# Kernel optimization log

Hardware: AMD Instinct MI355X
Metric: run time of the kernel (lower is better)

## Reference

```python
import jax, jax.numpy as jnp
import numpy as np

N, E, F_IN, C, H = 50000, 800000, 256, 64, 2  # nodes, edges, in-feat, per-head dim, heads
NEG_SLOPE_ATT = 0.2   # GATConv leaky_relu slope
NEG_SLOPE = 0.01      # F.leaky_relu default
BN_EPS = 1e-5


def setup_inputs() -> dict:
    key = jax.random.key(0)
    ks = jax.random.split(key, 10)
    x = jax.random.normal(ks[0], (N, F_IN), dtype=jnp.float32)
    edge_index = jax.random.randint(ks[1], (2, E), 0, N, dtype=jnp.int32)
    # GATConv params
    W = jax.random.normal(ks[2], (F_IN, H * C), dtype=jnp.float32) / np.sqrt(F_IN)
    att_src = jax.random.normal(ks[3], (H, C), dtype=jnp.float32) / np.sqrt(C)
    att_dst = jax.random.normal(ks[4], (H, C), dtype=jnp.float32) / np.sqrt(C)
    conv_bias = jnp.zeros((H * C,), dtype=jnp.float32)
    # fc1: in = hidden*2*2 = 256, out = hidden = 64
    fc1_w = jax.random.normal(ks[5], (H * C * 2, C), dtype=jnp.float32) / np.sqrt(H * C * 2)
    fc1_b = jnp.zeros((C,), dtype=jnp.float32)
    bn_gamma = jnp.ones((C,), dtype=jnp.float32)
    bn_beta = jnp.zeros((C,), dtype=jnp.float32)
    bn_mean = jnp.zeros((C,), dtype=jnp.float32)
    bn_var = jnp.ones((C,), dtype=jnp.float32)
    fc2_w = jax.random.normal(ks[6], (C, 3), dtype=jnp.float32) / np.sqrt(C)
    fc2_b = jnp.zeros((3,), dtype=jnp.float32)
    return {"x": x, "edge_index": edge_index, "W": W, "att_src": att_src,
            "att_dst": att_dst, "conv_bias": conv_bias, "fc1_w": fc1_w, "fc1_b": fc1_b,
            "bn_gamma": bn_gamma, "bn_beta": bn_beta, "bn_mean": bn_mean,
            "bn_var": bn_var, "fc2_w": fc2_w, "fc2_b": fc2_b}


def gat_conv(x, edge_index, W, att_src, att_dst, bias):
    # Project: [N, H, C]
    h = (x @ W).reshape(N, H, C)
    a_s = jnp.einsum('nhc,hc->nh', h, att_src)  # [N, H]
    a_d = jnp.einsum('nhc,hc->nh', h, att_dst)
    # add self-loops (PyG default)
    loops = jnp.arange(N, dtype=edge_index.dtype)
    src = jnp.concatenate([edge_index[0], loops])
    dst = jnp.concatenate([edge_index[1], loops])
    e = jax.nn.leaky_relu(a_s[src] + a_d[dst], NEG_SLOPE_ATT)  # [E+N, H]
    # segment softmax over incoming edges of each dst node
    m = jax.ops.segment_max(e, dst, num_segments=N)
    e_exp = jnp.exp(e - m[dst])
    denom = jax.ops.segment_sum(e_exp, dst, num_segments=N)
    alpha = e_exp / denom[dst]  # [E+N, H]
    msg = h[src] * alpha[:, :, None]  # [E+N, H, C]
    out = jax.ops.segment_sum(msg, dst, num_segments=N)  # [N, H, C]
    return out.reshape(N, H * C) + bias


def reference(x, edge_index, W, att_src, att_dst, conv_bias, fc1_w, fc1_b,
              bn_gamma, bn_beta, bn_mean, bn_var, fc2_w, fc2_b):
    # eval mode: dropout = identity, BN uses running stats
    h = gat_conv(x, edge_index, W, att_src, att_dst, conv_bias)
    h = jax.nn.leaky_relu(h, NEG_SLOPE)
    edge_rep = jnp.concatenate([h[edge_index[0]], h[edge_index[1]]], axis=1)  # [E, 256]
    y = edge_rep @ fc1_w + fc1_b
    y = (y - bn_mean) * jax.lax.rsqrt(bn_var + BN_EPS) * bn_gamma + bn_beta
    y = jax.nn.leaky_relu(y, NEG_SLOPE)
    return y @ fc2_w + fc2_b  # [E, 3]
```

## Files before the change

### kernel.cpp

```cpp
#include <hip/hip_runtime.h>
#include <hip/hip_bf16.h>

#define N_NODES 50000
#define N_EDGES 800000
#define F_IN    256
#define C_DIM   64
#define HC      128
#define NPG     6250
#define NBB     32
#define NBLK    196

typedef __attribute__((ext_vector_type(8))) short bf16x8;
typedef __attribute__((ext_vector_type(4))) float f32x4;

static constexpr size_t OFF_HBF   = 0;
static constexpr size_t OFF_H2    = 12800000;
static constexpr size_t OFF_AB    = 25600000;
static constexpr size_t OFF_AS    = 38400000;
static constexpr size_t OFF_AD    = 38800000;
static constexpr size_t OFF_OFFS  = 39200000;
static constexpr size_t OFF_TOT   = 39400064;
static constexpr size_t OFF_CUR   = 39600064;
static constexpr size_t OFF_PART  = 39800064;
static constexpr size_t OFF_CSR2  = 39801088;
static constexpr size_t OFF_WT    = 46201088;
static constexpr size_t OFF_FC1T  = 46266624;
static constexpr size_t OFF_SCALE = 46299392;
static constexpr size_t OFF_CC    = 46299904;
static constexpr size_t OFF_FC2M  = 46300416;
static constexpr size_t OFF_BCNT  = 46302464;
static constexpr size_t OFF_BASE  = 52702464;

__device__ __forceinline__ float2 bf2(unsigned u) {
    float2 r;
    r.x = __uint_as_float(u << 16);
    r.y = __uint_as_float(u & 0xffff0000u);
    return r;
}
__device__ __forceinline__ unsigned short f2bf(float f) {
    unsigned u = __float_as_uint(f);
    return (unsigned short)((u + 0x7fffu + ((u >> 16) & 1u)) >> 16);
}
__device__ __forceinline__ short f2bf_s(float f) {
    __hip_bfloat16 h = __float2bfloat16(f);
    return *reinterpret_cast<short*>(&h);
}

__global__ __launch_bounds__(256) void k_prep(const float* __restrict__ W,
                                              const float* __restrict__ fc1,
                                              const float* __restrict__ fc1_b,
                                              const float* __restrict__ gamma,
                                              const float* __restrict__ beta,
                                              const float* __restrict__ mean,
                                              const float* __restrict__ var,
                                              const float* __restrict__ fc2_w,
                                              unsigned short* __restrict__ Wt,
                                              unsigned short* __restrict__ fc1t,
                                              float* __restrict__ scale,
                                              float* __restrict__ cc,
                                              unsigned short* __restrict__ fc2m) {
    int id = blockIdx.x * 256 + threadIdx.x;
    if (id < 32768) {
        int n = id >> 8, k = id & 255;
        Wt[id] = f2bf(W[k * HC + n]);
    }
    int id2 = id - 32768;
    if (id2 >= 0 && id2 < 16384) {
        int j = id2 >> 7, q = id2 & 127;
        int L = q >> 1, b = q & 1;
        int kch = 32 * (L >> 4) + (L & 15) + 16 * b;
        float v = (j < 64) ? fc1[kch * 64 + j] : fc1[(128 + kch) * 64 + (j - 64)];
        fc1t[id2] = f2bf(v);
    }
    int id3 = id - (32768 + 16384);
    if (id3 >= 0 && id3 < 128) {
        int jj = id3 & 63;
        float s = gamma[jj] * rsqrtf(var[jj] + 1e-5f);
        scale[id3] = s;
        cc[id3] = (id3 < 64) ? 0.f : (fc1_b[jj] - mean[jj]) * s + beta[jj];
    }
    int id4 = id - (32768 + 16384 + 128);
    if (id4 >= 0 && id4 < 1024) {
        int kk = id4 >> 9, rem = id4 & 511;
        int lane = rem >> 3, j = rem & 7;
        int q  = kk * 16 + (lane >> 4) * 4 + (j >> 1);
        int ch = 32 * (q >> 4) + (q & 15) + 16 * (j & 1);
        int col = lane & 15;
        float v = (col < 3) ? fc2_w[ch * 3 + col] : 0.f;
        fc2m[id4] = f2bf(v);
    }
}

__global__ __launch_bounds__(256) void k_hist(const int* __restrict__ dst,
                                              int* __restrict__ bcnt) {
    __shared__ int hist[NPG];
    const int g  = blockIdx.x & 7;
    const int bi = blockIdx.x >> 3;
    const int lo = g * NPG, hi = lo + NPG;
    for (int j = threadIdx.x; j < NPG; j += 256) hist[j] = 0;
    __syncthreads();
    const int4* d4 = (const int4*)dst + bi * 6250;
#pragma unroll 1
    for (int it = 0; it < 25; ++it) {
        int idx = it * 256 + threadIdx.x;
        if (idx < 6250) {
            int4 d = d4[idx];
            if (d.x >= lo && d.x < hi) atomicAdd(&hist[d.x - lo], 1);
            if (d.y >= lo && d.y < hi) atomicAdd(&hist[d.y - lo], 1);
            if (d.z >= lo && d.z < hi) atomicAdd(&hist[d.z - lo], 1);
            if (d.w >= lo && d.w < hi) atomicAdd(&hist[d.w - lo], 1);
        }
    }
    __syncthreads();
    int* row = bcnt + (size_t)(g * NBB + bi) * NPG;
    for (int j = threadIdx.x; j < NPG; j += 256) row[j] = hist[j];
}

__global__ void k_tot(const int* __restrict__ bcnt, int* __restrict__ tot) {
    int n = blockIdx.x * 256 + threadIdx.x;
    if (n >= N_NODES) return;
    int g = n / NPG, ln = n - g * NPG;
    const int* col = bcnt + (size_t)g * NBB * NPG + ln;
    int s = 0;
#pragma unroll
    for (int bi = 0; bi < NBB; ++bi) s += col[bi * NPG];
    tot[n] = s;
}

__global__ void k_scan_part(const int* __restrict__ deg, int* __restrict__ part) {
    __shared__ int sd[256];
    int i = blockIdx.x * 256 + threadIdx.x;
    sd[threadIdx.x] = (i < N_NODES) ? deg[i] : 0;
    __syncthreads();
    for (int off = 128; off > 0; off >>= 1) {
        if (threadIdx.x < off) sd[threadIdx.x] += sd[threadIdx.x + off];
        __syncthreads();
    }
    if (threadIdx.x == 0) part[blockIdx.x] = sd[0];
}

__global__ void k_scan_final(const int* __restrict__ deg, const int* __restrict__ part,
                             int* __restrict__ offs) {
    __shared__ int sp[256];
    __shared__ int sd[256];
    const int t = threadIdx.x;
    int pv = (t < NBLK && t < (int)blockIdx.x) ? part[t] : 0;
    sp[t] = pv;
    __syncthreads();
    for (int off = 128; off > 0; off >>= 1) {
        if (t < off) sp[t] += sp[t + off];
        __syncthreads();
    }
    const int base = sp[0];
    __syncthreads();
    int i = blockIdx.x * 256 + t;
    int v = (i < N_NODES) ? deg[i] : 0;
    sd[t] = v;
    __syncthreads();
    for (int off = 1; off < 256; off <<= 1) {
        int u = (t >= off) ? sd[t - off] : 0;
        __syncthreads();
        sd[t] += u;
        __syncthreads();
    }
    if (i < N_NODES) {
        int o = base + sd[t] - v;
        offs[i] = o;
        if (i == N_NODES - 1) offs[N_NODES] = o + v;
    }
}

__global__ void k_base(const int* __restrict__ bcnt, const int* __restrict__ offs,
                       int* __restrict__ base) {
    int n = blockIdx.x * 256 + threadIdx.x;
    if (n >= N_NODES) return;
    int g = n / NPG, ln = n - g * NPG;
    const int* col = bcnt + (size_t)g * NBB * NPG + ln;
    int* bcol = base + (size_t)g * NBB * NPG + ln;
    int run = offs[n];
#pragma unroll
    for (int bi = 0; bi < NBB; ++bi) {
        bcol[bi * NPG] = run;
        run += col[bi * NPG];
    }
}

__global__ __launch_bounds__(256) void k_scatter(const int* __restrict__ src,
                                                 const int* __restrict__ dst,
                                                 const int* __restrict__ base,
                                                 int2* __restrict__ csr2) {
    __shared__ int cnt[NPG];
    const int g  = blockIdx.x & 7;
    const int bi = blockIdx.x >> 3;
    const int lo = g * NPG, hi = lo + NPG;
    const int* brow = base + (size_t)(g * NBB + bi) * NPG;
    for (int j = threadIdx.x; j < NPG; j += 256) cnt[j] = brow[j];
    __syncthreads();
    const int4* d4 = (const int4*)dst + bi * 6250;
    const int4* s4 = (const int4*)src + bi * 6250;
    const int ebase = bi * 25000;
#pragma unroll 1
    for (int it = 0; it < 25; ++it) {
        int idx = it * 256 + threadIdx.x;
        if (idx < 6250) {
            int4 d = d4[idx];
            int4 s = s4[idx];
            int e = ebase + idx * 4;
            if (d.x >= lo && d.x < hi) { int p = atomicAdd(&cnt[d.x - lo], 1); csr2[p] = make_int2(s.x, e);     }
            if (d.y >= lo && d.y < hi) { int p = atomicAdd(&cnt[d.y - lo], 1); csr2[p] = make_int2(s.y, e + 1); }
            if (d.z >= lo && d.z < hi) { int p = atomicAdd(&cnt[d.z - lo], 1); csr2[p] = make_int2(s.z, e + 2); }
            if (d.w >= lo && d.w < hi) { int p = atomicAdd(&cnt[d.w - lo], 1); csr2[p] = make_int2(s.w, e + 3); }
        }
    }
}

__global__ __launch_bounds__(256, 4) void k_mfma_xw(const float* __restrict__ x,
                                                    const unsigned short* __restrict__ Wt,
                                                    const float* __restrict__ att_src,
                                                    const float* __restrict__ att_dst,
                                                    unsigned* __restrict__ h_p,
                                                    float* __restrict__ as_,
                                                    float* __restrict__ ad_) {
    __shared__ float xs[16 * 256];
    __shared__ float sAs[16][2], sAd[16][2];
    const int t    = threadIdx.x;
    const int v    = t >> 6;
    const int lane = t & 63;
    const int c16  = lane & 15;
    const int kg   = lane >> 4;
    const int r0   = blockIdx.x * 16;
    if (t < 32) { ((float*)sAs)[t] = 0.f; ((float*)sAd)[t] = 0.f; }

    {
        const float4* xsrc = (const float4*)(x + (size_t)r0 * F_IN);
        float4* xsl = (float4*)xs;
#pragma unroll
        for (int it = 0; it < 4; ++it) {
            int cidx = it * 256 + t;
            int rl = cidx >> 6, j = cidx & 63;
            float4 val = xsrc[cidx];
            xsl[rl * 64 + (j ^ rl)] = val;
        }
    }
    const int cf0 = 2 * v, cf1 = 2 * v + 1;
    bf16x8 wf0[8], wf1[8];
#pragma unroll
    for (int kk = 0; kk < 8; ++kk) {
        wf0[kk] = *(const bf16x8*)(Wt + (size_t)(cf0 * 16 + c16) * 256 + kk * 32 + kg * 8);
        wf1[kk] = *(const bf16x8*)(Wt + (size_t)(cf1 * 16 + c16) * 256 + kk * 32 + kg * 8);
    }
    __syncthreads();

    f32x4 acc0 = {}, acc1 = {};
#pragma unroll
    for (int kk = 0; kk < 8; ++kk) {
        int j0 = kk * 8 + kg * 2;
        float4 a0 = *(const float4*)(xs + (size_t)(c16 * 64 + (j0 ^ c16)) * 4);
        float4 a1 = *(const float4*)(xs + (size_t)(c16 * 64 + ((j0 + 1) ^ c16)) * 4);
        float fv[8] = {a0.x, a0.y, a0.z, a0.w, a1.x, a1.y, a1.z, a1.w};
        bf16x8 ahi, alo;
#pragma unroll
        for (int q = 0; q < 8; ++q) {
            unsigned u = __float_as_uint(fv[q]);
            float hval = __uint_as_float(u & 0xffff0000u);
            float d = fv[q] - hval;
            ahi[q] = (short)(u >> 16);
            alo[q] = (short)(__float_as_uint(d) >> 16);
        }
        acc0 = __builtin_amdgcn_mfma_f32_16x16x32_bf16(alo, wf0[kk], acc0, 0, 0, 0);
        acc0 = __builtin_amdgcn_mfma_f32_16x16x32_bf16(ahi, wf0[kk], acc0, 0, 0, 0);
        acc1 = __builtin_amdgcn_mfma_f32_16x16x32_bf16(alo, wf1[kk], acc1, 0, 0, 0);
        acc1 = __builtin_amdgcn_mfma_f32_16x16x32_bf16(ahi, wf1[kk], acc1, 0, 0, 0);
    }
#pragma unroll
    for (int i = 0; i < 4; ++i) {
        int row = r0 + kg * 4 + i;
        unsigned pu = (unsigned)f2bf(acc0[i]) | ((unsigned)f2bf(acc1[i]) << 16);
        h_p[(size_t)row * 64 + v * 16 + c16] = pu;
    }
    float ws0 = att_src[cf0 * 16 + c16], ws1 = att_src[cf1 * 16 + c16];
    float wd0 = att_dst[cf0 * 16 + c16], wd1 = att_dst[cf1 * 16 + c16];
    float pas[4], pad[4];
#pragma unroll
    for (int i = 0; i < 4; ++i) {
        pas[i] = acc0[i] * ws0 + acc1[i] * ws1;
        pad[i] = acc0[i] * wd0 + acc1[i] * wd1;
    }
#pragma unroll
    for (int m = 1; m < 16; m <<= 1) {
#pragma unroll
        for (int i = 0; i < 4; ++i) {
            pas[i] += __shfl_xor(pas[i], m, 64);
            pad[i] += __shfl_xor(pad[i], m, 64);
        }
    }
    const int head = v >> 1;
    if (c16 == 0) {
#pragma unroll
        for (int i = 0; i < 4; ++i) {
            atomicAdd(&sAs[kg * 4 + i][head], pas[i]);
            atomicAdd(&sAd[kg * 4 + i][head], pad[i]);
        }
    }
    __syncthreads();
    if (t < 32) {
        int row = t >> 1, hd = t & 1;
        as_[(r0 + row) * 2 + hd] = sAs[row][hd];
        ad_[(r0 + row) * 2 + hd] = sAd[row][hd];
    }
}

__global__ __launch_bounds__(256) void k_agg(const unsigned* __restrict__ h_p,
                                             const float* __restrict__ as_,
                                             const float* __restrict__ ad_,
                                             const int* __restrict__ offs,
                                             const int2* __restrict__ csr2,
                                             const float* __restrict__ conv_bias,
                                             unsigned* __restrict__ h2_p) {
    const int n    = blockIdx.x * 4 + (threadIdx.x >> 6);
    const int lane = threadIdx.x & 63;
    const int ql   = lane & 15;
    const int q    = lane >> 4;
    const int hd   = ql >> 3;
    const float adn = ad_[n * 2 + hd];
    const uint4* h4 = (const uint4*)h_p;
    float a[8] = {};
    float accw = 0.f;
    const int beg = offs[n], end = offs[n + 1];
    int i = beg + q;
    for (; i + 4 < end; i += 8) {
        int s0 = csr2[i].x;
        int s1 = csr2[i + 4].x;
        uint4 u0 = h4[(unsigned)(s0 * 16 + ql)];
        uint4 u1 = h4[(unsigned)(s1 * 16 + ql)];
        float l0 = as_[s0 * 2 + hd] + adn;
        float l1 = as_[s1 * 2 + hd] + adn;
        l0 = fmaxf(l0, 0.2f * l0);
        l1 = fmaxf(l1, 0.2f * l1);
        float w0 = __expf(l0), w1 = __expf(l1);
        float2 t;
        t = bf2(u0.x); a[0] += w0 * t.x; a[1] += w0 * t.y;
        t = bf2(u0.y); a[2] += w0 * t.x; a[3] += w0 * t.y;
        t = bf2(u0.z); a[4] += w0 * t.x; a[5] += w0 * t.y;
        t = bf2(u0.w); a[6] += w0 * t.x; a[7] += w0 * t.y;
        t = bf2(u1.x); a[0] += w1 * t.x; a[1] += w1 * t.y;
        t = bf2(u1.y); a[2] += w1 * t.x; a[3] += w1 * t.y;
        t = bf2(u1.z); a[4] += w1 * t.x; a[5] += w1 * t.y;
        t = bf2(u1.w); a[6] += w1 * t.x; a[7] += w1 * t.y;
        accw += w0 + w1;
    }
    if (i < end) {
        int s0 = csr2[i].x;
        uint4 u0 = h4[(unsigned)(s0 * 16 + ql)];
        float l0 = as_[s0 * 2 + hd] + adn;
        l0 = fmaxf(l0, 0.2f * l0);
        float w0 = __expf(l0);
        float2 t;
        t = bf2(u0.x); a[0] += w0 * t.x; a[1] += w0 * t.y;
        t = bf2(u0.y); a[2] += w0 * t.x; a[3] += w0 * t.y;
        t = bf2(u0.z); a[4] += w0 * t.x; a[5] += w0 * t.y;
        t = bf2(u0.w); a[6] += w0 * t.x; a[7] += w0 * t.y;
        accw += w0;
    }
#pragma unroll
    for (int m = 16; m < 64; m <<= 1) {
#pragma unroll
        for (int j = 0; j < 8; ++j) a[j] += __shfl_xor(a[j], m, 64);
        accw += __shfl_xor(accw, m, 64);
    }
    if (q == 0) {
        float es = as_[n * 2 + hd] + adn;
        es = fmaxf(es, 0.2f * es);
        float wsl = __expf(es);
        uint4 un = h4[(unsigned)(n * 16 + ql)];
        float2 t;
        t = bf2(un.x); a[0] += wsl * t.x; a[1] += wsl * t.y;
        t = bf2(un.y); a[2] += wsl * t.x; a[3] += wsl * t.y;
        t = bf2(un.z); a[4] += wsl * t.x; a[5] += wsl * t.y;
        t = bf2(un.w); a[6] += wsl * t.x; a[7] += wsl * t.y;
        accw += wsl;
        float rinv = 1.f / accw;
        unsigned pw[4];
#pragma unroll
        for (int j = 0; j < 4; ++j) {
            int w = 4 * ql + j;
            int c = 32 * (w >> 4) + (w & 15);
            float o0 = a[2 * j] * rinv + conv_bias[c];
            float o1 = a[2 * j + 1] * rinv + conv_bias[c + 16];
            o0 = fmaxf(o0, 0.01f * o0);
            o1 = fmaxf(o1, 0.01f * o1);
            pw[j] = (unsigned)f2bf(o0) | ((unsigned)f2bf(o1) << 16);
        }
        ((uint4*)h2_p)[(unsigned)(n * 16 + ql)] = make_uint4(pw[0], pw[1], pw[2], pw[3]);
    }
}

__global__ __launch_bounds__(256) void k_mfma_uv(const unsigned short* __restrict__ h2,
                                                 const unsigned short* __restrict__ fc1t,
                                                 const float* __restrict__ scale,
                                                 const float* __restrict__ cc,
                                                 unsigned* __restrict__ ab_p) {
    const int w = blockIdx.x * 4 + (threadIdx.x >> 6);
    if (w >= N_NODES / 16) return;
    const int lane = threadIdx.x & 63;
    const int c16  = lane & 15;
    const int kg   = lane >> 4;
    const int r0   = w * 16;
    const unsigned short* arow = h2 + (size_t)(r0 + c16) * HC + kg * 8;
    bf16x8 af[4];
#pragma unroll
    for (int kk = 0; kk < 4; ++kk) af[kk] = *(const bf16x8*)(arow + kk * 32);
    f32x4 acc[8] = {};
#pragma unroll
    for (int kk = 0; kk < 4; ++kk) {
        const unsigned short* wp = fc1t + c16 * HC + kk * 32 + kg * 8;
#pragma unroll
        for (int cf = 0; cf < 8; ++cf) {
            bf16x8 b = *(const bf16x8*)(wp + cf * 16 * HC);
            acc[cf] = __builtin_amdgcn_mfma_f32_16x16x32_bf16(af[kk], b, acc[cf], 0, 0, 0);
        }
    }
#pragma unroll
    for (int cf = 0; cf < 8; cf += 2) {
        int j0 = cf * 16 + c16, j1 = j0 + 16;
        float s0 = scale[j0], s1 = scale[j1];
        float q0 = cc[j0],    q1 = cc[j1];
#pragma unroll
        for (int i = 0; i < 4; ++i) {
            int row = r0 + kg * 4 + i;
            unsigned pu = (unsigned)f2bf(acc[cf][i] * s0 + q0)
                        | ((unsigned)f2bf(acc[cf + 1][i] * s1 + q1) << 16);
            ab_p[(size_t)row * 64 + (cf >> 1) * 16 + c16] = pu;
        }
    }
}

__device__ __forceinline__ void mk_afrag(uint4 ua, const float* bb, bf16x8& ap) {
    float2 t; float z;
    t = bf2(ua.x);
    z = t.x + bb[0]; z = fmaxf(z, 0.01f * z); ap[0] = f2bf_s(z);
    z = t.y + bb[1]; z = fmaxf(z, 0.01f * z); ap[1] = f2bf_s(z);
    t = bf2(ua.y);
    z = t.x + bb[2]; z = fmaxf(z, 0.01f * z); ap[2] = f2bf_s(z);
    z = t.y + bb[3]; z = fmaxf(z, 0.01f * z); ap[3] = f2bf_s(z);
    t = bf2(ua.z);
    z = t.x + bb[4]; z = fmaxf(z, 0.01f * z); ap[4] = f2bf_s(z);
    z = t.y + bb[5]; z = fmaxf(z, 0.01f * z); ap[5] = f2bf_s(z);
    t = bf2(ua.w);
    z = t.x + bb[6]; z = fmaxf(z, 0.01f * z); ap[6] = f2bf_s(z);
    z = t.y + bb[7]; z = fmaxf(z, 0.01f * z); ap[7] = f2bf_s(z);
}

__global__ __launch_bounds__(256) void k_edge(const int* __restrict__ offs,
                                              const int2* __restrict__ csr2,
                                              const unsigned* __restrict__ ab_p,
                                              const unsigned short* __restrict__ fc2m,
                                              const float* __restrict__ fc2_b,
                                              float* __restrict__ out) {
    const int n    = blockIdx.x * 4 + (threadIdx.x >> 6);
    const int lane = threadIdx.x & 63;
    const int c16  = lane & 15;
    const int kg   = lane >> 4;
    bf16x8 bfr0 = *(const bf16x8*)(fc2m + (size_t)lane * 8);
    bf16x8 bfr1 = *(const bf16x8*)(fc2m + (size_t)(64 + lane) * 8);
    const uint4* abv = (const uint4*)ab_p;
    uint4 ub0 = abv[(unsigned)(n * 16 + 8 + kg)];
    uint4 ub1 = abv[(unsigned)(n * 16 + 12 + kg)];
    float bb0[8], bb1[8];
    {
        float2 t;
        t = bf2(ub0.x); bb0[0] = t.x; bb0[1] = t.y;
        t = bf2(ub0.y); bb0[2] = t.x; bb0[3] = t.y;
        t = bf2(ub0.z); bb0[4] = t.x; bb0[5] = t.y;
        t = bf2(ub0.w); bb0[6] = t.x; bb0[7] = t.y;
        t = bf2(ub1.x); bb1[0] = t.x; bb1[1] = t.y;
        t = bf2(ub1.y); bb1[2] = t.x; bb1[3] = t.y;
        t = bf2(ub1.z); bb1[4] = t.x; bb1[5] = t.y;
        t = bf2(ub1.w); bb1[6] = t.x; bb1[7] = t.y;
    }
    const float ob = (c16 < 3) ? fc2_b[c16] : 0.f;
    const int beg = offs[n], end = offs[n + 1];
    for (int base = beg; base < end; base += 16) {
        int slot = base + c16;
        int2 ce = (slot < end) ? csr2[slot] : make_int2(0, 0);
        uint4 ua0 = abv[(unsigned)(ce.x * 16 + kg)];
        uint4 ua1 = abv[(unsigned)(ce.x * 16 + 4 + kg)];
        bf16x8 ap0, ap1;
        mk_afrag(ua0, bb0, ap0);
        mk_afrag(ua1, bb1, ap1);
        f32x4 acc = {};
        acc = __builtin_amdgcn_mfma_f32_16x16x32_bf16(ap0, bfr0, acc, 0, 0, 0);
        acc = __builtin_amdgcn_mfma_f32_16x16x32_bf16(ap1, bfr1, acc, 0, 0, 0);
#pragma unroll
        for (int i = 0; i < 4; ++i) {
            int eid = __shfl(ce.y, kg * 4 + i, 64);
            if (c16 < 3 && (base + kg * 4 + i) < end)
                out[(size_t)eid * 3 + c16] = acc[i] + ob;
        }
    }
}

extern "C" void kernel_launch(void* const* d_in, const int* in_sizes, int n_in,
                              void* d_out, int out_size, void* d_ws, size_t ws_size,
                              hipStream_t stream) {
    const float* x        = (const float*)d_in[0];
    const int*   ei       = (const int*)d_in[1];
    const float* W        = (const float*)d_in[2];
    const float* att_src  = (const float*)d_in[3];
    const float* att_dst  = (const float*)d_in[4];
    const float* conv_b   = (const float*)d_in[5];
    const float* fc1_w    = (const float*)d_in[6];
    const float* fc1_b    = (const float*)d_in[7];
    const float* gamma    = (const float*)d_in[8];
    const float* beta     = (const float*)d_in[9];
    const float* mean     = (const float*)d_in[10];
    const float* var      = (const float*)d_in[11];
    const float* fc2_w    = (const float*)d_in[12];
    const float* fc2_b    = (const float*)d_in[13];
    float*       out      = (float*)d_out;
    char*        ws       = (char*)d_ws;

    const int* src = ei;
    const int* dst = ei + N_EDGES;

    unsigned*       h_p   = (unsigned*)(ws + OFF_HBF);
    unsigned*       h2_p  = (unsigned*)(ws + OFF_H2);
    unsigned*       ab_p  = (unsigned*)(ws + OFF_AB);
    float*          as_   = (float*)(ws + OFF_AS);
    float*          ad_   = (float*)(ws + OFF_AD);
    int*            offs  = (int*)(ws + OFF_OFFS);
    int*            tot   = (int*)(ws + OFF_TOT);
    int*            part  = (int*)(ws + OFF_PART);
    int2*           csr2  = (int2*)(ws + OFF_CSR2);
    unsigned short* Wt    = (unsigned short*)(ws + OFF_WT);
    unsigned short* fc1t  = (unsigned short*)(ws + OFF_FC1T);
    float*          scale = (float*)(ws + OFF_SCALE);
    float*          cc    = (float*)(ws + OFF_CC);
    unsigned short* fc2m  = (unsigned short*)(ws + OFF_FC2M);
    int*            bcnt  = (int*)(ws + OFF_BCNT);
    int*            base  = (int*)(ws + OFF_BASE);

    k_prep<<<235, 256, 0, stream>>>(W, fc1_w, fc1_b, gamma, beta, mean, var, fc2_w,
                                    Wt, fc1t, scale, cc, fc2m);

    k_hist      <<<8 * NBB, 256, 0, stream>>>(dst, bcnt);
    k_tot       <<<NBLK, 256, 0, stream>>>(bcnt, tot);
    k_scan_part <<<NBLK, 256, 0, stream>>>(tot, part);
    k_scan_final<<<NBLK, 256, 0, stream>>>(tot, part, offs);
    k_base      <<<NBLK, 256, 0, stream>>>(bcnt, offs, base);
    k_scatter   <<<8 * NBB, 256, 0, stream>>>(src, dst, base, csr2);

    k_mfma_xw<<<N_NODES / 16, 256, 0, stream>>>(x, Wt, att_src, att_dst, h_p, as_, ad_);
    k_agg    <<<N_NODES / 4, 256, 0, stream>>>(h_p, as_, ad_, offs, csr2, conv_b, h2_p);
    k_mfma_uv<<<(N_NODES / 16 + 3) / 4, 256, 0, stream>>>((const unsigned short*)h2_p, fc1t, scale, cc, ab_p);

    k_edge<<<N_NODES / 4, 256, 0, stream>>>(offs, csr2, ab_p, fc2m, fc2_b, out);
}
```

Measured before the change: 172.2 us.

## Merge histogram into XW GEMM launch and fuse scan kernels

The edge-destination histogram blocks are folded into the XW projection kernel as extra blocks of a single launch, so the two independent stages can run concurrently on the GPU. The total-degree reduction is merged with the partial-scan kernel, and the per-bucket base computation is merged with the final scan. Together these cut the launch count from 8 to 4 for this front section and remove intermediate kernel boundaries. The trade-off is a heterogeneous kernel whose shared-memory footprint is the larger of the two roles, which may lower occupancy for the GEMM blocks.

```diff
diff --git a/kernel.cpp b/kernel.cpp
--- a/kernel.cpp
+++ b/kernel.cpp
@@ -9,6 +9,8 @@
 #define NPG     6250
 #define NBB     32
 #define NBLK    196
+#define XW_BLOCKS   3125
+#define HIST_BLOCKS 256
 
 typedef __attribute__((ext_vector_type(8))) short bf16x8;
 typedef __attribute__((ext_vector_type(4))) float f32x4;
@@ -20,7 +22,6 @@
 static constexpr size_t OFF_AD    = 38800000;
 static constexpr size_t OFF_OFFS  = 39200000;
 static constexpr size_t OFF_TOT   = 39400064;
-static constexpr size_t OFF_CUR   = 39600064;
 static constexpr size_t OFF_PART  = 39800064;
 static constexpr size_t OFF_CSR2  = 39801088;
 static constexpr size_t OFF_WT    = 46201088;
@@ -91,46 +92,145 @@
     }
 }
 
-__global__ __launch_bounds__(256) void k_hist(const int* __restrict__ dst,
-                                              int* __restrict__ bcnt) {
-    __shared__ int hist[NPG];
-    const int g  = blockIdx.x & 7;
-    const int bi = blockIdx.x >> 3;
-    const int lo = g * NPG, hi = lo + NPG;
-    for (int j = threadIdx.x; j < NPG; j += 256) hist[j] = 0;
-    __syncthreads();
-    const int4* d4 = (const int4*)dst + bi * 6250;
+__global__ __launch_bounds__(256, 4) void k_front(const float* __restrict__ x,
+                                                  const unsigned short* __restrict__ Wt,
+                                                  const float* __restrict__ att_src,
+                                                  const float* __restrict__ att_dst,
+                                                  unsigned* __restrict__ h_p,
+                                                  float* __restrict__ as_,
+                                                  float* __restrict__ ad_,
+                                                  const int* __restrict__ dst,
+                                                  int* __restrict__ bcnt) {
+    __shared__ int smem[6464];
+    const int t = threadIdx.x;
+
+    if (blockIdx.x >= XW_BLOCKS) {
+        int* hist = smem;
+        const int bid = blockIdx.x - XW_BLOCKS;
+        const int g  = bid & 7;
+        const int bi = bid >> 3;
+        const int lo = g * NPG, hi = lo + NPG;
+        for (int j = t; j < NPG; j += 256) hist[j] = 0;
+        __syncthreads();
+        const int4* d4 = (const int4*)dst + bi * 6250;
 #pragma unroll 1
-    for (int it = 0; it < 25; ++it) {
-        int idx = it * 256 + threadIdx.x;
-        if (idx < 6250) {
-            int4 d = d4[idx];
-            if (d.x >= lo && d.x < hi) atomicAdd(&hist[d.x - lo], 1);
-            if (d.y >= lo && d.y < hi) atomicAdd(&hist[d.y - lo], 1);
-            if (d.z >= lo && d.z < hi) atomicAdd(&hist[d.z - lo], 1);
-            if (d.w >= lo && d.w < hi) atomicAdd(&hist[d.w - lo], 1);
-        }
-    }
-    __syncthreads();
-    int* row = bcnt + (size_t)(g * NBB + bi) * NPG;
-    for (int j = threadIdx.x; j < NPG; j += 256) row[j] = hist[j];
-}
-
-__global__ void k_tot(const int* __restrict__ bcnt, int* __restrict__ tot) {
+        for (int it = 0; it < 25; ++it) {
+            int idx = it * 256 + t;
+            if (idx < 6250) {
+                int4 d = d4[idx];
+                if (d.x >= lo && d.x < hi) atomicAdd(&hist[d.x - lo], 1);
+                if (d.y >= lo && d.y < hi) atomicAdd(&hist[d.y - lo], 1);
+                if (d.z >= lo && d.z < hi) atomicAdd(&hist[d.z - lo], 1);
+                if (d.w >= lo && d.w < hi) atomicAdd(&hist[d.w - lo], 1);
+            }
+        }
+        __syncthreads();
+        int* row = bcnt + (size_t)(g * NBB + bi) * NPG;
+        for (int j = t; j < NPG; j += 256) row[j] = hist[j];
+        return;
+    }
+
+    float* xs  = (float*)smem;
+    float* sAs = (float*)(smem + 4096);
+    float* sAd = sAs + 32;
+    const int v    = t >> 6;
+    const int lane = t & 63;
+    const int c16  = lane & 15;
+    const int kg   = lane >> 4;
+    const int r0   = blockIdx.x * 16;
+    if (t < 32) { sAs[t] = 0.f; sAd[t] = 0.f; }
+    {
+        const float4* xsrc = (const float4*)(x + (size_t)r0 * F_IN);
+        float4* xsl = (float4*)xs;
+#pragma unroll
+        for (int it = 0; it < 4; ++it) {
+            int cidx = it * 256 + t;
+            int rl = cidx >> 6, j = cidx & 63;
+            float4 val = xsrc[cidx];
+            xsl[rl * 64 + (j ^ rl)] = val;
+        }
+    }
+    const int cf0 = 2 * v, cf1 = 2 * v + 1;
+    bf16x8 wf0[8], wf1[8];
+#pragma unroll
+    for (int kk = 0; kk < 8; ++kk) {
+        wf0[kk] = *(const bf16x8*)(Wt + (size_t)(cf0 * 16 + c16) * 256 + kk * 32 + kg * 8);
+        wf1[kk] = *(const bf16x8*)(Wt + (size_t)(cf1 * 16 + c16) * 256 + kk * 32 + kg * 8);
+    }
+    __syncthreads();
+
+    f32x4 acc0 = {}, acc1 = {};
+#pragma unroll
+    for (int kk = 0; kk < 8; ++kk) {
+        int j0 = kk * 8 + kg * 2;
+        float4 a0 = *(const float4*)(xs + (size_t)(c16 * 64 + (j0 ^ c16)) * 4);
+        float4 a1 = *(const float4*)(xs + (size_t)(c16 * 64 + ((j0 + 1) ^ c16)) * 4);
+        float fv[8] = {a0.x, a0.y, a0.z, a0.w, a1.x, a1.y, a1.z, a1.w};
+        bf16x8 ahi, alo;
+#pragma unroll
+        for (int q = 0; q < 8; ++q) {
+            unsigned u = __float_as_uint(fv[q]);
+            float hval = __uint_as_float(u & 0xffff0000u);
+            float d = fv[q] - hval;
+            ahi[q] = (short)(u >> 16);
+            alo[q] = (short)(__float_as_uint(d) >> 16);
+        }
+        acc0 = __builtin_amdgcn_mfma_f32_16x16x32_bf16(alo, wf0[kk], acc0, 0, 0, 0);
+        acc0 = __builtin_amdgcn_mfma_f32_16x16x32_bf16(ahi, wf0[kk], acc0, 0, 0, 0);
+        acc1 = __builtin_amdgcn_mfma_f32_16x16x32_bf16(alo, wf1[kk], acc1, 0, 0, 0);
+        acc1 = __builtin_amdgcn_mfma_f32_16x16x32_bf16(ahi, wf1[kk], acc1, 0, 0, 0);
+    }
+#pragma unroll
+    for (int i = 0; i < 4; ++i) {
+        int row = r0 + kg * 4 + i;
+        unsigned pu = (unsigned)f2bf(acc0[i]) | ((unsigned)f2bf(acc1[i]) << 16);
+        h_p[(size_t)row * 64 + v * 16 + c16] = pu;
+    }
+    float ws0 = att_src[cf0 * 16 + c16], ws1 = att_src[cf1 * 16 + c16];
+    float wd0 = att_dst[cf0 * 16 + c16], wd1 = att_dst[cf1 * 16 + c16];
+    float pas[4], pad[4];
+#pragma unroll
+    for (int i = 0; i < 4; ++i) {
+        pas[i] = acc0[i] * ws0 + acc1[i] * ws1;
+        pad[i] = acc0[i] * wd0 + acc1[i] * wd1;
+    }
+#pragma unroll
+    for (int m = 1; m < 16; m <<= 1) {
+#pragma unroll
+        for (int i = 0; i < 4; ++i) {
+            pas[i] += __shfl_xor(pas[i], m, 64);
+            pad[i] += __shfl_xor(pad[i], m, 64);
+        }
+    }
+    const int head = v >> 1;
+    if (c16 == 0) {
+#pragma unroll
+        for (int i = 0; i < 4; ++i) {
+            atomicAdd(&sAs[(kg * 4 + i) * 2 + head], pas[i]);
+            atomicAdd(&sAd[(kg * 4 + i) * 2 + head], pad[i]);
+        }
+    }
+    __syncthreads();
+    if (t < 32) {
+        int row = t >> 1, hd = t & 1;
+        as_[(r0 + row) * 2 + hd] = sAs[row * 2 + hd];
+        ad_[(r0 + row) * 2 + hd] = sAd[row * 2 + hd];
+    }
+}
+
+__global__ void k_tot_part(const int* __restrict__ bcnt, int* __restrict__ tot,
+                           int* __restrict__ part) {
+    __shared__ int sd[256];
     int n = blockIdx.x * 256 + threadIdx.x;
-    if (n >= N_NODES) return;
-    int g = n / NPG, ln = n - g * NPG;
-    const int* col = bcnt + (size_t)g * NBB * NPG + ln;
     int s = 0;
-#pragma unroll
-    for (int bi = 0; bi < NBB; ++bi) s += col[bi * NPG];
-    tot[n] = s;
-}
-
-__global__ void k_scan_part(const int* __restrict__ deg, int* __restrict__ part) {
-    __shared__ int sd[256];
-    int i = blockIdx.x * 256 + threadIdx.x;
-    sd[threadIdx.x] = (i < N_NODES) ? deg[i] : 0;
+    if (n < N_NODES) {
+        int g = n / NPG, ln = n - g * NPG;
+        const int* col = bcnt + (size_t)g * NBB * NPG + ln;
+#pragma unroll
+        for (int bi = 0; bi < NBB; ++bi) s += col[bi * NPG];
+        tot[n] = s;
+    }
+    sd[threadIdx.x] = s;
     __syncthreads();
     for (int off = 128; off > 0; off >>= 1) {
         if (threadIdx.x < off) sd[threadIdx.x] += sd[threadIdx.x + off];
@@ -139,8 +239,9 @@
     if (threadIdx.x == 0) part[blockIdx.x] = sd[0];
 }
 
-__global__ void k_scan_final(const int* __restrict__ deg, const int* __restrict__ part,
-                             int* __restrict__ offs) {
+__global__ void k_scan_base(const int* __restrict__ tot, const int* __restrict__ part,
+                            const int* __restrict__ bcnt, int* __restrict__ offs,
+                            int* __restrict__ base) {
     __shared__ int sp[256];
     __shared__ int sd[256];
     const int t = threadIdx.x;
@@ -151,10 +252,10 @@
         if (t < off) sp[t] += sp[t + off];
         __syncthreads();
     }
-    const int base = sp[0];
+    const int bb = sp[0];
     __syncthreads();
     int i = blockIdx.x * 256 + t;
-    int v = (i < N_NODES) ? deg[i] : 0;
+    int v = (i < N_NODES) ? tot[i] : 0;
     sd[t] = v;
     __syncthreads();
     for (int off = 1; off < 256; off <<= 1) {
@@ -164,24 +265,18 @@
         __syncthreads();
     }
     if (i < N_NODES) {
-        int o = base + sd[t] - v;
+        int o = bb + sd[t] - v;
         offs[i] = o;
         if (i == N_NODES - 1) offs[N_NODES] = o + v;
-    }
-}
-
-__global__ void k_base(const int* __restrict__ bcnt, const int* __restrict__ offs,
-                       int* __restrict__ base) {
-    int n = blockIdx.x * 256 + threadIdx.x;
-    if (n >= N_NODES) return;
-    int g = n / NPG, ln = n - g * NPG;
-    const int* col = bcnt + (size_t)g * NBB * NPG + ln;
-    int* bcol = base + (size_t)g * NBB * NPG + ln;
-    int run = offs[n];
-#pragma unroll
-    for (int bi = 0; bi < NBB; ++bi) {
-        bcol[bi * NPG] = run;
-        run += col[bi * NPG];
+        int g = i / NPG, ln = i - g * NPG;
+        const int* col = bcnt + (size_t)g * NBB * NPG + ln;
+        int* bcol = base + (size_t)g * NBB * NPG + ln;
+        int run = o;
+#pragma unroll
+        for (int bi = 0; bi < NBB; ++bi) {
+            bcol[bi * NPG] = run;
+            run += col[bi * NPG];
+        }
     }
 }
 
@@ -211,102 +306,6 @@
             if (d.z >= lo && d.z < hi) { int p = atomicAdd(&cnt[d.z - lo], 1); csr2[p] = make_int2(s.z, e + 2); }
             if (d.w >= lo && d.w < hi) { int p = atomicAdd(&cnt[d.w - lo], 1); csr2[p] = make_int2(s.w, e + 3); }
         }
-    }
-}
-
-__global__ __launch_bounds__(256, 4) void k_mfma_xw(const float* __restrict__ x,
-                                                    const unsigned short* __restrict__ Wt,
-                                                    const float* __restrict__ att_src,
-                                                    const float* __restrict__ att_dst,
-                                                    unsigned* __restrict__ h_p,
-                                                    float* __restrict__ as_,
-                                                    float* __restrict__ ad_) {
-    __shared__ float xs[16 * 256];
-    __shared__ float sAs[16][2], sAd[16][2];
-    const int t    = threadIdx.x;
-    const int v    = t >> 6;
-    const int lane = t & 63;
-    const int c16  = lane & 15;
-    const int kg   = lane >> 4;
-    const int r0   = blockIdx.x * 16;
-    if (t < 32) { ((float*)sAs)[t] = 0.f; ((float*)sAd)[t] = 0.f; }
-
-    {
-        const float4* xsrc = (const float4*)(x + (size_t)r0 * F_IN);
-        float4* xsl = (float4*)xs;
-#pragma unroll
-        for (int it = 0; it < 4; ++it) {
-            int cidx = it * 256 + t;
-            int rl = cidx >> 6, j = cidx & 63;
-            float4 val = xsrc[cidx];
-            xsl[rl * 64 + (j ^ rl)] = val;
-        }
-    }
-    const int cf0 = 2 * v, cf1 = 2 * v + 1;
-    bf16x8 wf0[8], wf1[8];
-#pragma unroll
-    for (int kk = 0; kk < 8; ++kk) {
-        wf0[kk] = *(const bf16x8*)(Wt + (size_t)(cf0 * 16 + c16) * 256 + kk * 32 + kg * 8);
-        wf1[kk] = *(const bf16x8*)(Wt + (size_t)(cf1 * 16 + c16) * 256 + kk * 32 + kg * 8);
-    }
-    __syncthreads();
-
-    f32x4 acc0 = {}, acc1 = {};
-#pragma unroll
-    for (int kk = 0; kk < 8; ++kk) {
-        int j0 = kk * 8 + kg * 2;
-        float4 a0 = *(const float4*)(xs + (size_t)(c16 * 64 + (j0 ^ c16)) * 4);
-        float4 a1 = *(const float4*)(xs + (size_t)(c16 * 64 + ((j0 + 1) ^ c16)) * 4);
-        float fv[8] = {a0.x, a0.y, a0.z, a0.w, a1.x, a1.y, a1.z, a1.w};
-        bf16x8 ahi, alo;
-#pragma unroll
-        for (int q = 0; q < 8; ++q) {
-            unsigned u = __float_as_uint(fv[q]);
-            float hval = __uint_as_float(u & 0xffff0000u);
-            float d = fv[q] - hval;
-            ahi[q] = (short)(u >> 16);
-            alo[q] = (short)(__float_as_uint(d) >> 16);
-        }
-        acc0 = __builtin_amdgcn_mfma_f32_16x16x32_bf16(alo, wf0[kk], acc0, 0, 0, 0);
-        acc0 = __builtin_amdgcn_mfma_f32_16x16x32_bf16(ahi, wf0[kk], acc0, 0, 0, 0);
-        acc1 = __builtin_amdgcn_mfma_f32_16x16x32_bf16(alo, wf1[kk], acc1, 0, 0, 0);
-        acc1 = __builtin_amdgcn_mfma_f32_16x16x32_bf16(ahi, wf1[kk], acc1, 0, 0, 0);
-    }
-#pragma unroll
-    for (int i = 0; i < 4; ++i) {
-        int row = r0 + kg * 4 + i;
-        unsigned pu = (unsigned)f2bf(acc0[i]) | ((unsigned)f2bf(acc1[i]) << 16);
-        h_p[(size_t)row * 64 + v * 16 + c16] = pu;
-    }
-    float ws0 = att_src[cf0 * 16 + c16], ws1 = att_src[cf1 * 16 + c16];
-    float wd0 = att_dst[cf0 * 16 + c16], wd1 = att_dst[cf1 * 16 + c16];
-    float pas[4], pad[4];
-#pragma unroll
-    for (int i = 0; i < 4; ++i) {
-        pas[i] = acc0[i] * ws0 + acc1[i] * ws1;
-        pad[i] = acc0[i] * wd0 + acc1[i] * wd1;
-    }
-#pragma unroll
-    for (int m = 1; m < 16; m <<= 1) {
-#pragma unroll
-        for (int i = 0; i < 4; ++i) {
-            pas[i] += __shfl_xor(pas[i], m, 64);
-            pad[i] += __shfl_xor(pad[i], m, 64);
-        }
-    }
-    const int head = v >> 1;
-    if (c16 == 0) {
-#pragma unroll
-        for (int i = 0; i < 4; ++i) {
-            atomicAdd(&sAs[kg * 4 + i][head], pas[i]);
-            atomicAdd(&sAd[kg * 4 + i][head], pad[i]);
-        }
-    }
-    __syncthreads();
-    if (t < 32) {
-        int row = t >> 1, hd = t & 1;
-        as_[(r0 + row) * 2 + hd] = sAs[row][hd];
-        ad_[(r0 + row) * 2 + hd] = sAd[row][hd];
     }
 }
 
@@ -543,16 +542,14 @@
     k_prep<<<235, 256, 0, stream>>>(W, fc1_w, fc1_b, gamma, beta, mean, var, fc2_w,
                                     Wt, fc1t, scale, cc, fc2m);
 
-    k_hist      <<<8 * NBB, 256, 0, stream>>>(dst, bcnt);
-    k_tot       <<<NBLK, 256, 0, stream>>>(bcnt, tot);
-    k_scan_part <<<NBLK, 256, 0, stream>>>(tot, part);
-    k_scan_final<<<NBLK, 256, 0, stream>>>(tot, part, offs);
-    k_base      <<<NBLK, 256, 0, stream>>>(bcnt, offs, base);
-    k_scatter   <<<8 * NBB, 256, 0, stream>>>(src, dst, base, csr2);
-
-    k_mfma_xw<<<N_NODES / 16, 256, 0, stream>>>(x, Wt, att_src, att_dst, h_p, as_, ad_);
+    k_front<<<XW_BLOCKS + HIST_BLOCKS, 256, 0, stream>>>(x, Wt, att_src, att_dst,
+                                                         h_p, as_, ad_, dst, bcnt);
+
+    k_tot_part <<<NBLK, 256, 0, stream>>>(bcnt, tot, part);
+    k_scan_base<<<NBLK, 256, 0, stream>>>(tot, part, bcnt, offs, base);
+    k_scatter  <<<8 * NBB, 256, 0, stream>>>(src, dst, base, csr2);
+
     k_agg    <<<N_NODES / 4, 256, 0, stream>>>(h_p, as_, ad_, offs, csr2, conv_b, h2_p);
     k_mfma_uv<<<(N_NODES / 16 + 3) / 4, 256, 0, stream>>>((const unsigned short*)h2_p, fc1t, scale, cc, ab_p);
-
-    k_edge<<<N_NODES / 4, 256, 0, stream>>>(offs, csr2, ab_p, fc2m, fc2_b, out);
-}
+    k_edge   <<<N_NODES / 4, 256, 0, stream>>>(offs, csr2, ab_p, fc2m, fc2_b, out);
+}
```

Measured after the change: 165.3 us. 4.0% less time.
